# Kernel tuning notes

Measured on AMD Instinct MI355X. Metric: run time of the kernel, lower is better.

The kernel has to match this reference:

```python
import jax, jax.numpy as jnp
import numpy as np

N_HEADS = 32
N_KV_HEADS = 8
DIM = 4096
HEAD_DIM = DIM // N_HEADS  # 128
N_REP = N_HEADS // N_KV_HEADS  # 4
MAX_B = 4
CACHE_LEN = 1024
SEQ = 1024
BATCH = 4


def _rope(t, cos, sin):
    # t: (b, s, h, hd); interpret last dim as interleaved complex pairs
    tr = t[..., 0::2]
    ti = t[..., 1::2]
    cos = cos[None, :, None, :]
    sin = sin[None, :, None, :]
    out_r = tr * cos - ti * sin
    out_i = tr * sin + ti * cos
    return jnp.stack([out_r, out_i], axis=-1).reshape(t.shape)


def setup_inputs() -> dict:
    key = jax.random.key(0)
    ks = jax.random.split(key, 6)
    x = jax.random.normal(ks[0], (BATCH, SEQ, DIM), dtype=jnp.float32)
    wq = jax.random.normal(ks[1], (DIM, N_HEADS * HEAD_DIM), dtype=jnp.float32) * (DIM ** -0.5)
    wk = jax.random.normal(ks[2], (DIM, N_KV_HEADS * HEAD_DIM), dtype=jnp.float32) * (DIM ** -0.5)
    wv = jax.random.normal(ks[3], (DIM, N_KV_HEADS * HEAD_DIM), dtype=jnp.float32) * (DIM ** -0.5)
    wo = jax.random.normal(ks[4], (DIM, DIM), dtype=jnp.float32) * (DIM ** -0.5)
    # standard RoPE frequencies, theta = 10000
    inv_freq = 1.0 / (10000.0 ** (np.arange(0, HEAD_DIM, 2, dtype=np.float32) / HEAD_DIM))
    pos = np.arange(SEQ, dtype=np.float32)
    ang = np.outer(pos, inv_freq)  # (SEQ, HEAD_DIM/2)
    freqs_cos = jnp.asarray(np.cos(ang), dtype=jnp.float32)
    freqs_sin = jnp.asarray(np.sin(ang), dtype=jnp.float32)
    return {"x": x, "freqs_cos": freqs_cos, "freqs_sin": freqs_sin,
            "wq": wq, "wk": wk, "wv": wv, "wo": wo, "start": 0}


def reference(x, freqs_cos, freqs_sin, wq, wk, wv, wo, start):
    b, s, _ = x.shape
    xq = (x @ wq).reshape(b, s, N_HEADS, HEAD_DIM)
    xk = (x @ wk).reshape(b, s, N_KV_HEADS, HEAD_DIM)
    xv = (x @ wv).reshape(b, s, N_KV_HEADS, HEAD_DIM)

    xq = _rope(xq, freqs_cos, freqs_sin)
    xk = _rope(xk, freqs_cos, freqs_sin)

    # KV cache append (cache initialized to zeros as in the module)
    cache_k = jnp.zeros((MAX_B, CACHE_LEN, N_KV_HEADS, HEAD_DIM), dtype=x.dtype)
    cache_v = jnp.zeros((MAX_B, CACHE_LEN, N_KV_HEADS, HEAD_DIM), dtype=x.dtype)
    cache_k = cache_k.at[:b, start:start + s].set(xk)
    cache_v = cache_v.at[:b, start:start + s].set(xv)

    keys = cache_k[:b, :start + s]    # (b, kv, n_kv, hd)
    values = cache_v[:b, :start + s]

    # repeat_kv to match query heads (GQA)
    keys = jnp.repeat(keys, N_REP, axis=2)      # (b, kv, n_q, hd)
    values = jnp.repeat(values, N_REP, axis=2)

    scale = 1.0 / jnp.sqrt(jnp.float32(HEAD_DIM)).astype(x.dtype)
    scores = jnp.einsum('bqhd,bkhd->bhqk', xq, keys) * scale
    probs = jax.nn.softmax(scores, axis=-1)
    out = jnp.einsum('bhqk,bkhd->bqhd', probs, values).reshape(b, s, DIM)
    return out @ wo
```

## Files before the change

### kernel.cpp

```cpp
#include <hip/hip_runtime.h>
#include <cstdint>

#define B_SZ 4
#define S_LEN 1024
#define DIM 4096
#define NH 32
#define KVH 8
#define HD 128
#define DQKV 6144

typedef __bf16 bf16x8 __attribute__((ext_vector_type(8)));
typedef float f32x4 __attribute__((ext_vector_type(4)));

__device__ __forceinline__ unsigned short f2bf(float f) {
  union { float f; uint32_t u; } v; v.f = f;
  uint32_t u = v.u;
  return (unsigned short)((u + 0x7fffu + ((u >> 16) & 1u)) >> 16);
}
__device__ __forceinline__ float bf2f(unsigned short h) {
  union { uint32_t u; float f; } v; v.u = ((uint32_t)h) << 16;
  return v.f;
}

__device__ __forceinline__ void async16(void* lds, const void* g) {
  __builtin_amdgcn_global_load_lds(
      (const __attribute__((address_space(1))) void*)g,
      (__attribute__((address_space(3))) void*)lds, 16, 0, 0);
}

__global__ void cvt_x_kernel(const float* __restrict__ x, unsigned short* __restrict__ xb) {
  size_t i = ((size_t)blockIdx.x * 256 + threadIdx.x) * 4;
  float4 v = *(const float4*)(x + i);
  ushort4 o;
  o.x = f2bf(v.x); o.y = f2bf(v.y); o.z = f2bf(v.z); o.w = f2bf(v.w);
  *(ushort4*)(xb + i) = o;
}

__global__ void wtrans_kernel(const float* __restrict__ w, unsigned short* __restrict__ wt, int N) {
  __shared__ __align__(16) float tile[32][33];
  int n0 = blockIdx.x * 32, k0 = blockIdx.y * 32;
  int tx = threadIdx.x & 31, ty = threadIdx.x >> 5;
#pragma unroll
  for (int i = 0; i < 4; i++) {
    int k = ty + i * 8;
    tile[k][tx] = w[(size_t)(k0 + k) * N + n0 + tx];
  }
  __syncthreads();
#pragma unroll
  for (int i = 0; i < 4; i++) {
    int n = ty + i * 8;
    wt[(size_t)(n0 + n) * DIM + k0 + tx] = f2bf(tile[tx][n]);
  }
}

template <bool OUT_BF16>
__global__ __launch_bounds__(256, 2) void gemm_bt_kernel(
    const unsigned short* __restrict__ A, const unsigned short* __restrict__ Bt,
    void* __restrict__ Cout, int Kdim, int ldc) {
  __shared__ __align__(16) unsigned short lA[128 * 32];
  __shared__ __align__(16) unsigned short lB[128 * 32];
  const int tid = threadIdx.x;
  const int wave = tid >> 6, lane = tid & 63;
  const int m0 = blockIdx.y * 128, n0 = blockIdx.x * 128;
  const int r0 = tid >> 2, c0 = (tid & 3) * 8;
  const unsigned short* gA0 = A + (size_t)(m0 + r0) * Kdim + c0;
  const unsigned short* gA1 = gA0 + (size_t)64 * Kdim;
  const unsigned short* gB0 = Bt + (size_t)(n0 + r0) * Kdim + c0;
  const unsigned short* gB1 = gB0 + (size_t)64 * Kdim;
  unsigned short* lA0 = lA + wave * 512;
  unsigned short* lA1 = lA + 2048 + wave * 512;
  unsigned short* lB0 = lB + wave * 512;
  unsigned short* lB1 = lB + 2048 + wave * 512;
  const int wm = (wave & 1) * 64, wn = (wave >> 1) * 64;
  const int lql = lane & 15, lqh = lane >> 4;
  f32x4 acc[4][4] = {};
  for (int kk = 0; kk < Kdim; kk += 32) {
    __syncthreads();
    async16(lA0, gA0 + kk);
    async16(lA1, gA1 + kk);
    async16(lB0, gB0 + kk);
    async16(lB1, gB1 + kk);
    __syncthreads();
    bf16x8 af[4], bfr[4];
#pragma unroll
    for (int mi = 0; mi < 4; mi++)
      af[mi] = *(const bf16x8*)(lA + (wm + mi * 16 + lql) * 32 + lqh * 8);
#pragma unroll
    for (int ni = 0; ni < 4; ni++)
      bfr[ni] = *(const bf16x8*)(lB + (wn + ni * 16 + lql) * 32 + lqh * 8);
#pragma unroll
    for (int mi = 0; mi < 4; mi++)
#pragma unroll
      for (int ni = 0; ni < 4; ni++)
        acc[mi][ni] = __builtin_amdgcn_mfma_f32_16x16x32_bf16(af[mi], bfr[ni], acc[mi][ni], 0, 0, 0);
  }
#pragma unroll
  for (int mi = 0; mi < 4; mi++)
#pragma unroll
    for (int ni = 0; ni < 4; ni++)
#pragma unroll
      for (int r = 0; r < 4; r++) {
        int row = m0 + wm + mi * 16 + lqh * 4 + r;
        int col = n0 + wn + ni * 16 + lql;
        float v = acc[mi][ni][r];
        if (OUT_BF16)
          ((unsigned short*)Cout)[(size_t)row * ldc + col] = f2bf(v);
        else
          ((float*)Cout)[(size_t)row * ldc + col] = v;
      }
}

__global__ void rope_kernel(const unsigned short* __restrict__ src, const float* __restrict__ fc,
                            const float* __restrict__ fs, unsigned short* __restrict__ dst,
                            int nheads, float scale) {
  int idx = blockIdx.x * 256 + threadIdx.x;
  int f = idx & 63;
  int rest = idx >> 6;
  int hh = rest % nheads;
  int t = rest / nheads;
  int s = t & (S_LEN - 1);
  int b = t >> 10;
  const unsigned short* p = src + (size_t)t * DQKV + hh * HD + 2 * f;
  ushort2 xv = *(const ushort2*)p;
  float xr = bf2f(xv.x), xi = bf2f(xv.y);
  float c = fc[s * 64 + f], sn = fs[s * 64 + f];
  ushort2 o;
  o.x = f2bf((xr * c - xi * sn) * scale);
  o.y = f2bf((xr * sn + xi * c) * scale);
  *(ushort2*)(dst + ((size_t)(b * nheads + hh) * S_LEN + s) * HD + 2 * f) = o;
}

__global__ void vtrans_kernel(const unsigned short* __restrict__ src, unsigned short* __restrict__ Vt) {
  __shared__ __align__(16) unsigned short tile[32][33];
  int s0 = blockIdx.x * 32, d0 = blockIdx.y * 32, bk = blockIdx.z;
  int tx = threadIdx.x & 31, ty = threadIdx.x >> 5;
#pragma unroll
  for (int i = 0; i < 4; i++) {
    int s = ty + i * 8;
    tile[s][tx] = src[(size_t)((bk >> 3) * S_LEN + s0 + s) * DQKV + (bk & 7) * HD + d0 + tx];
  }
  __syncthreads();
#pragma unroll
  for (int i = 0; i < 4; i++) {
    int d = ty + i * 8;
    Vt[((size_t)bk * HD + d0 + d) * S_LEN + s0 + tx] = tile[tx][d];
  }
}

__global__ __launch_bounds__(256, 2) void attn_kernel(
    const unsigned short* __restrict__ Qb,
    const unsigned short* __restrict__ Kb,
    const unsigned short* __restrict__ Vt,
    unsigned short* __restrict__ Ob) {
  __shared__ __align__(16) unsigned short Kt[64][136];
  __shared__ __align__(16) unsigned short Vl[128][72];
  __shared__ __align__(16) unsigned short Pl[4][16][72];
  const int tid = threadIdx.x, wave = tid >> 6, lane = tid & 63;
  const int qb = blockIdx.x, h = blockIdx.y, b = blockIdx.z;
  const int kvh = h >> 2;
  const int lql = lane & 15, lqh = lane >> 4;
  const int qrow = qb * 64 + wave * 16;

  const unsigned short* Qp = Qb + ((size_t)(b * NH + h) * S_LEN + qrow + lql) * HD + lqh * 8;
  bf16x8 qf[4];
#pragma unroll
  for (int kd = 0; kd < 4; kd++) qf[kd] = *(const bf16x8*)(Qp + kd * 32);

  const unsigned short* Kp = Kb + (size_t)(b * KVH + kvh) * S_LEN * HD;
  const unsigned short* Vp = Vt + (size_t)(b * KVH + kvh) * HD * S_LEN;

  float m_run[4], l_run[4];
  f32x4 Oacc[8] = {};
#pragma unroll
  for (int r = 0; r < 4; r++) { m_run[r] = -3.0e38f; l_run[r] = 0.0f; }

  for (int kt = 0; kt < S_LEN; kt += 64) {
    __syncthreads();
#pragma unroll
    for (int i = 0; i < 4; i++) {
      int c = tid + 256 * i;
      int key = c >> 4, doff = (c & 15) * 8;
      *(uint4*)(&Kt[key][doff]) = *(const uint4*)(Kp + (size_t)(kt + key) * HD + doff);
    }
#pragma unroll
    for (int i = 0; i < 4; i++) {
      int c = tid + 256 * i;
      int d = c >> 3, koff = (c & 7) * 8;
      *(uint4*)(&Vl[d][koff]) = *(const uint4*)(Vp + (size_t)d * S_LEN + kt + koff);
    }
    __syncthreads();
    f32x4 sf[4] = {};
#pragma unroll
    for (int ni = 0; ni < 4; ni++)
#pragma unroll
      for (int kd = 0; kd < 4; kd++) {
        bf16x8 kf = *(const bf16x8*)(&Kt[ni * 16 + lql][kd * 32 + lqh * 8]);
        sf[ni] = __builtin_amdgcn_mfma_f32_16x16x32_bf16(qf[kd], kf, sf[ni], 0, 0, 0);
      }
    float mnew[4], alpha[4], psum[4];
#pragma unroll
    for (int r = 0; r < 4; r++) {
      float v = fmaxf(fmaxf(sf[0][r], sf[1][r]), fmaxf(sf[2][r], sf[3][r]));
      v = fmaxf(v, __shfl_xor(v, 1));
      v = fmaxf(v, __shfl_xor(v, 2));
      v = fmaxf(v, __shfl_xor(v, 4));
      v = fmaxf(v, __shfl_xor(v, 8));
      mnew[r] = fmaxf(m_run[r], v);
      alpha[r] = __expf(m_run[r] - mnew[r]);
      m_run[r] = mnew[r];
      psum[r] = 0.0f;
    }
#pragma unroll
    for (int ni = 0; ni < 4; ni++)
#pragma unroll
      for (int r = 0; r < 4; r++) {
        float p = __expf(sf[ni][r] - mnew[r]);
        psum[r] += p;
        Pl[wave][lqh * 4 + r][ni * 16 + lql] = f2bf(p);
      }
#pragma unroll
    for (int r = 0; r < 4; r++) {
      float v = psum[r];
      v += __shfl_xor(v, 1);
      v += __shfl_xor(v, 2);
      v += __shfl_xor(v, 4);
      v += __shfl_xor(v, 8);
      l_run[r] = l_run[r] * alpha[r] + v;
    }
#pragma unroll
    for (int ni = 0; ni < 8; ni++)
#pragma unroll
      for (int r = 0; r < 4; r++) Oacc[ni][r] *= alpha[r];
    bf16x8 pa[2];
#pragma unroll
    for (int ks = 0; ks < 2; ks++)
      pa[ks] = *(const bf16x8*)(&Pl[wave][lql][ks * 32 + lqh * 8]);
#pragma unroll
    for (int ni = 0; ni < 8; ni++)
#pragma unroll
      for (int ks = 0; ks < 2; ks++) {
        bf16x8 vb = *(const bf16x8*)(&Vl[ni * 16 + lql][ks * 32 + lqh * 8]);
        Oacc[ni] = __builtin_amdgcn_mfma_f32_16x16x32_bf16(pa[ks], vb, Oacc[ni], 0, 0, 0);
      }
  }
#pragma unroll
  for (int r = 0; r < 4; r++) l_run[r] = 1.0f / l_run[r];
#pragma unroll
  for (int ni = 0; ni < 8; ni++)
#pragma unroll
    for (int r = 0; r < 4; r++) {
      int q = qrow + lqh * 4 + r;
      Ob[(size_t)(b * S_LEN + q) * DIM + h * HD + ni * 16 + lql] = f2bf(Oacc[ni][r] * l_run[r]);
    }
}

extern "C" void kernel_launch(void* const* d_in, const int* in_sizes, int n_in,
                              void* d_out, int out_size, void* d_ws, size_t ws_size,
                              hipStream_t stream) {
  (void)in_sizes; (void)n_in; (void)out_size; (void)ws_size;
  const float* x  = (const float*)d_in[0];
  const float* fc = (const float*)d_in[1];
  const float* fs = (const float*)d_in[2];
  const float* wq = (const float*)d_in[3];
  const float* wk = (const float*)d_in[4];
  const float* wv = (const float*)d_in[5];
  const float* wo = (const float*)d_in[6];
  float* out = (float*)d_out;
  char* ws = (char*)d_ws;

  const size_t MB = 1024 * 1024;
  unsigned short* xb    = (unsigned short*)(ws + 0);
  unsigned short* attnb = (unsigned short*)(ws + 0);
  unsigned short* wqkvt = (unsigned short*)(ws + 32 * MB);
  unsigned short* Qb    = (unsigned short*)(ws + 32 * MB);
  unsigned short* Kb    = (unsigned short*)(ws + 64 * MB);
  unsigned short* Vt    = (unsigned short*)(ws + 72 * MB);
  unsigned short* wot   = (unsigned short*)(ws + 80 * MB);
  unsigned short* qkv   = (unsigned short*)(ws + 112 * MB);

  cvt_x_kernel<<<16384, 256, 0, stream>>>(x, xb);
  wtrans_kernel<<<dim3(128, 128), 256, 0, stream>>>(wq, wqkvt, 4096);
  wtrans_kernel<<<dim3(32, 128), 256, 0, stream>>>(wk, wqkvt + (size_t)4096 * 4096, 1024);
  wtrans_kernel<<<dim3(32, 128), 256, 0, stream>>>(wv, wqkvt + (size_t)5120 * 4096, 1024);
  wtrans_kernel<<<dim3(128, 128), 256, 0, stream>>>(wo, wot, 4096);
  gemm_bt_kernel<true><<<dim3(DQKV / 128, 32), 256, 0, stream>>>(xb, wqkvt, qkv, DIM, DQKV);
  rope_kernel<<<32768, 256, 0, stream>>>(qkv, fc, fs, Qb, NH, 0.08838834764831845f);
  rope_kernel<<<8192, 256, 0, stream>>>(qkv + 4096, fc, fs, Kb, KVH, 1.0f);
  vtrans_kernel<<<dim3(32, 4, 32), 256, 0, stream>>>(qkv + 5120, Vt);
  attn_kernel<<<dim3(16, NH, B_SZ), 256, 0, stream>>>(Qb, Kb, Vt, attnb);
  gemm_bt_kernel<false><<<dim3(32, 32), 256, 0, stream>>>(attnb, wot, out, DIM, DIM);
}
```

Before: 886.9 us.

## Swizzle LDS layouts, async-load attention tiles, vectorize rope and weight transpose

Applies XOR swizzles to the GEMM and attention LDS tiles so reads avoid bank conflicts without padding. K and V tiles are now filled with direct global-to-LDS async loads. Softmax switches to exp2 with log2(e) folded into the Q scale, and P is truncated to bf16 instead of rounded. Rope is vectorized to 16-byte accesses, the weight transpose uses 64x64 tiles with paired stores, and attention occupancy is raised to 3 blocks. The truncation slightly changes numerics and the swizzles must match the load layout exactly.

After: 804.2 us. 9.3% less time.

```diff
diff --git a/kernel.cpp b/kernel.cpp
--- a/kernel.cpp
+++ b/kernel.cpp
@@ -21,6 +21,13 @@
   union { uint32_t u; float f; } v; v.u = ((uint32_t)h) << 16;
   return v.f;
 }
+__device__ __forceinline__ float ex2(float x) {
+#if __has_builtin(__builtin_amdgcn_exp2f)
+  return __builtin_amdgcn_exp2f(x);
+#else
+  return exp2f(x);
+#endif
+}
 
 __device__ __forceinline__ void async16(void* lds, const void* g) {
   __builtin_amdgcn_global_load_lds(
@@ -37,19 +44,23 @@
 }
 
 __global__ void wtrans_kernel(const float* __restrict__ w, unsigned short* __restrict__ wt, int N) {
-  __shared__ __align__(16) float tile[32][33];
-  int n0 = blockIdx.x * 32, k0 = blockIdx.y * 32;
-  int tx = threadIdx.x & 31, ty = threadIdx.x >> 5;
-#pragma unroll
-  for (int i = 0; i < 4; i++) {
-    int k = ty + i * 8;
+  __shared__ float tile[64][65];
+  int n0 = blockIdx.x * 64, k0 = blockIdx.y * 64;
+  int tx = threadIdx.x & 63, ty = threadIdx.x >> 6;
+#pragma unroll
+  for (int i = 0; i < 16; i++) {
+    int k = ty + i * 4;
     tile[k][tx] = w[(size_t)(k0 + k) * N + n0 + tx];
   }
   __syncthreads();
-#pragma unroll
-  for (int i = 0; i < 4; i++) {
-    int n = ty + i * 8;
-    wt[(size_t)(n0 + n) * DIM + k0 + tx] = f2bf(tile[tx][n]);
+  int c = threadIdx.x & 31, ny = threadIdx.x >> 5;
+#pragma unroll
+  for (int i = 0; i < 8; i++) {
+    int n = ny + i * 8;
+    ushort2 o;
+    o.x = f2bf(tile[2 * c][n]);
+    o.y = f2bf(tile[2 * c + 1][n]);
+    *(ushort2*)(wt + (size_t)(n0 + n) * DIM + k0 + 2 * c) = o;
   }
 }
 
@@ -62,7 +73,8 @@
   const int tid = threadIdx.x;
   const int wave = tid >> 6, lane = tid & 63;
   const int m0 = blockIdx.y * 128, n0 = blockIdx.x * 128;
-  const int r0 = tid >> 2, c0 = (tid & 3) * 8;
+  const int r0 = tid >> 2;
+  const int c0 = ((tid & 3) ^ ((tid >> 3) & 3)) * 8;
   const unsigned short* gA0 = A + (size_t)(m0 + r0) * Kdim + c0;
   const unsigned short* gA1 = gA0 + (size_t)64 * Kdim;
   const unsigned short* gB0 = Bt + (size_t)(n0 + r0) * Kdim + c0;
@@ -73,6 +85,7 @@
   unsigned short* lB1 = lB + 2048 + wave * 512;
   const int wm = (wave & 1) * 64, wn = (wave >> 1) * 64;
   const int lql = lane & 15, lqh = lane >> 4;
+  const int ksw = (lqh ^ ((lql >> 1) & 3)) * 8;
   f32x4 acc[4][4] = {};
   for (int kk = 0; kk < Kdim; kk += 32) {
     __syncthreads();
@@ -84,10 +97,10 @@
     bf16x8 af[4], bfr[4];
 #pragma unroll
     for (int mi = 0; mi < 4; mi++)
-      af[mi] = *(const bf16x8*)(lA + (wm + mi * 16 + lql) * 32 + lqh * 8);
+      af[mi] = *(const bf16x8*)(lA + (wm + mi * 16 + lql) * 32 + ksw);
 #pragma unroll
     for (int ni = 0; ni < 4; ni++)
-      bfr[ni] = *(const bf16x8*)(lB + (wn + ni * 16 + lql) * 32 + lqh * 8);
+      bfr[ni] = *(const bf16x8*)(lB + (wn + ni * 16 + lql) * 32 + ksw);
 #pragma unroll
     for (int mi = 0; mi < 4; mi++)
 #pragma unroll
@@ -112,22 +125,27 @@
 
 __global__ void rope_kernel(const unsigned short* __restrict__ src, const float* __restrict__ fc,
                             const float* __restrict__ fs, unsigned short* __restrict__ dst,
-                            int nheads, float scale) {
+                            int nheads, int hshift, float scale) {
   int idx = blockIdx.x * 256 + threadIdx.x;
-  int f = idx & 63;
-  int rest = idx >> 6;
-  int hh = rest % nheads;
-  int t = rest / nheads;
+  int f4 = idx & 15;
+  int rest = idx >> 4;
+  int hh = rest & (nheads - 1);
+  int t = rest >> hshift;
   int s = t & (S_LEN - 1);
   int b = t >> 10;
-  const unsigned short* p = src + (size_t)t * DQKV + hh * HD + 2 * f;
-  ushort2 xv = *(const ushort2*)p;
-  float xr = bf2f(xv.x), xi = bf2f(xv.y);
-  float c = fc[s * 64 + f], sn = fs[s * 64 + f];
-  ushort2 o;
-  o.x = f2bf((xr * c - xi * sn) * scale);
-  o.y = f2bf((xr * sn + xi * c) * scale);
-  *(ushort2*)(dst + ((size_t)(b * nheads + hh) * S_LEN + s) * HD + 2 * f) = o;
+  union { uint4 v; unsigned short u[8]; } in, out;
+  in.v = *(const uint4*)(src + (size_t)t * DQKV + hh * HD + f4 * 8);
+  union { float4 v; float f[4]; } c4, s4;
+  c4.v = *(const float4*)(fc + s * 64 + f4 * 4);
+  s4.v = *(const float4*)(fs + s * 64 + f4 * 4);
+#pragma unroll
+  for (int j = 0; j < 4; j++) {
+    float xr = bf2f(in.u[2 * j]), xi = bf2f(in.u[2 * j + 1]);
+    float cc = c4.f[j], ss = s4.f[j];
+    out.u[2 * j] = f2bf((xr * cc - xi * ss) * scale);
+    out.u[2 * j + 1] = f2bf((xr * ss + xi * cc) * scale);
+  }
+  *(uint4*)(dst + ((size_t)(b * nheads + hh) * S_LEN + s) * HD + f4 * 8) = out.v;
 }
 
 __global__ void vtrans_kernel(const unsigned short* __restrict__ src, unsigned short* __restrict__ Vt) {
@@ -147,13 +165,13 @@
   }
 }
 
-__global__ __launch_bounds__(256, 2) void attn_kernel(
+__global__ __launch_bounds__(256, 3) void attn_kernel(
     const unsigned short* __restrict__ Qb,
     const unsigned short* __restrict__ Kb,
     const unsigned short* __restrict__ Vt,
     unsigned short* __restrict__ Ob) {
-  __shared__ __align__(16) unsigned short Kt[64][136];
-  __shared__ __align__(16) unsigned short Vl[128][72];
+  __shared__ __align__(16) unsigned short Kt[64][128];
+  __shared__ __align__(16) unsigned short Vl[128][64];
   __shared__ __align__(16) unsigned short Pl[4][16][72];
   const int tid = threadIdx.x, wave = tid >> 6, lane = tid & 63;
   const int qb = blockIdx.x, h = blockIdx.y, b = blockIdx.z;
@@ -168,6 +186,10 @@
 
   const unsigned short* Kp = Kb + (size_t)(b * KVH + kvh) * S_LEN * HD;
   const unsigned short* Vp = Vt + (size_t)(b * KVH + kvh) * HD * S_LEN;
+  const int krow_in = lane >> 4;
+  const int kcol_sw = lane & 15;
+  const int vrow_in = lane >> 3;
+  const int vcol_off = ((lane & 7) ^ (lane >> 3)) * 8;
 
   float m_run[4], l_run[4];
   f32x4 Oacc[8] = {};
@@ -177,26 +199,28 @@
   for (int kt = 0; kt < S_LEN; kt += 64) {
     __syncthreads();
 #pragma unroll
-    for (int i = 0; i < 4; i++) {
-      int c = tid + 256 * i;
-      int key = c >> 4, doff = (c & 15) * 8;
-      *(uint4*)(&Kt[key][doff]) = *(const uint4*)(Kp + (size_t)(kt + key) * HD + doff);
-    }
-#pragma unroll
-    for (int i = 0; i < 4; i++) {
-      int c = tid + 256 * i;
-      int d = c >> 3, koff = (c & 7) * 8;
-      *(uint4*)(&Vl[d][koff]) = *(const uint4*)(Vp + (size_t)d * S_LEN + kt + koff);
+    for (int j = 0; j < 4; j++) {
+      int rbase = wave * 16 + j * 4;
+      int r = rbase + krow_in;
+      async16(&Kt[rbase][0], Kp + (size_t)(kt + r) * HD + ((kcol_sw ^ (r & 7)) * 8));
+    }
+#pragma unroll
+    for (int j = 0; j < 4; j++) {
+      int dbase = wave * 32 + j * 8;
+      int d = dbase + vrow_in;
+      async16(&Vl[dbase][0], Vp + (size_t)d * S_LEN + kt + vcol_off);
     }
     __syncthreads();
     f32x4 sf[4] = {};
 #pragma unroll
-    for (int ni = 0; ni < 4; ni++)
+    for (int ni = 0; ni < 4; ni++) {
+      const int ksw = lql & 7;
 #pragma unroll
       for (int kd = 0; kd < 4; kd++) {
-        bf16x8 kf = *(const bf16x8*)(&Kt[ni * 16 + lql][kd * 32 + lqh * 8]);
+        bf16x8 kf = *(const bf16x8*)(&Kt[ni * 16 + lql][((kd * 4 + lqh) ^ ksw) * 8]);
         sf[ni] = __builtin_amdgcn_mfma_f32_16x16x32_bf16(qf[kd], kf, sf[ni], 0, 0, 0);
       }
+    }
     float mnew[4], alpha[4], psum[4];
 #pragma unroll
     for (int r = 0; r < 4; r++) {
@@ -206,7 +230,7 @@
       v = fmaxf(v, __shfl_xor(v, 4));
       v = fmaxf(v, __shfl_xor(v, 8));
       mnew[r] = fmaxf(m_run[r], v);
-      alpha[r] = __expf(m_run[r] - mnew[r]);
+      alpha[r] = ex2(m_run[r] - mnew[r]);
       m_run[r] = mnew[r];
       psum[r] = 0.0f;
     }
@@ -214,9 +238,10 @@
     for (int ni = 0; ni < 4; ni++)
 #pragma unroll
       for (int r = 0; r < 4; r++) {
-        float p = __expf(sf[ni][r] - mnew[r]);
+        float p = ex2(sf[ni][r] - mnew[r]);
         psum[r] += p;
-        Pl[wave][lqh * 4 + r][ni * 16 + lql] = f2bf(p);
+        union { float f; uint32_t u; } pv; pv.f = p;
+        Pl[wave][lqh * 4 + r][ni * 16 + lql] = (unsigned short)(pv.u >> 16);
       }
 #pragma unroll
     for (int r = 0; r < 4; r++) {
@@ -236,12 +261,14 @@
     for (int ks = 0; ks < 2; ks++)
       pa[ks] = *(const bf16x8*)(&Pl[wave][lql][ks * 32 + lqh * 8]);
 #pragma unroll
-    for (int ni = 0; ni < 8; ni++)
+    for (int ni = 0; ni < 8; ni++) {
+      const int ksw = lql & 7;
 #pragma unroll
       for (int ks = 0; ks < 2; ks++) {
-        bf16x8 vb = *(const bf16x8*)(&Vl[ni * 16 + lql][ks * 32 + lqh * 8]);
+        bf16x8 vb = *(const bf16x8*)(&Vl[ni * 16 + lql][((ks * 4 + lqh) ^ ksw) * 8]);
         Oacc[ni] = __builtin_amdgcn_mfma_f32_16x16x32_bf16(pa[ks], vb, Oacc[ni], 0, 0, 0);
       }
+    }
   }
 #pragma unroll
   for (int r = 0; r < 4; r++) l_run[r] = 1.0f / l_run[r];
@@ -279,13 +306,13 @@
   unsigned short* qkv   = (unsigned short*)(ws + 112 * MB);
 
   cvt_x_kernel<<<16384, 256, 0, stream>>>(x, xb);
-  wtrans_kernel<<<dim3(128, 128), 256, 0, stream>>>(wq, wqkvt, 4096);
-  wtrans_kernel<<<dim3(32, 128), 256, 0, stream>>>(wk, wqkvt + (size_t)4096 * 4096, 1024);
-  wtrans_kernel<<<dim3(32, 128), 256, 0, stream>>>(wv, wqkvt + (size_t)5120 * 4096, 1024);
-  wtrans_kernel<<<dim3(128, 128), 256, 0, stream>>>(wo, wot, 4096);
+  wtrans_kernel<<<dim3(64, 64), 256, 0, stream>>>(wq, wqkvt, 4096);
+  wtrans_kernel<<<dim3(16, 64), 256, 0, stream>>>(wk, wqkvt + (size_t)4096 * 4096, 1024);
+  wtrans_kernel<<<dim3(16, 64), 256, 0, stream>>>(wv, wqkvt + (size_t)5120 * 4096, 1024);
+  wtrans_kernel<<<dim3(64, 64), 256, 0, stream>>>(wo, wot, 4096);
   gemm_bt_kernel<true><<<dim3(DQKV / 128, 32), 256, 0, stream>>>(xb, wqkvt, qkv, DIM, DQKV);
-  rope_kernel<<<32768, 256, 0, stream>>>(qkv, fc, fs, Qb, NH, 0.08838834764831845f);
-  rope_kernel<<<8192, 256, 0, stream>>>(qkv + 4096, fc, fs, Kb, KVH, 1.0f);
+  rope_kernel<<<8192, 256, 0, stream>>>(qkv, fc, fs, Qb, NH, 5, 0.12751879505099168f);
+  rope_kernel<<<2048, 256, 0, stream>>>(qkv + 4096, fc, fs, Kb, KVH, 3, 1.0f);
   vtrans_kernel<<<dim3(32, 4, 32), 256, 0, stream>>>(qkv + 5120, Vt);
   attn_kernel<<<dim3(16, NH, B_SZ), 256, 0, stream>>>(Qb, Kb, Vt, attnb);
   gemm_bt_kernel<false><<<dim3(32, 32), 256, 0, stream>>>(attnb, wot, out, DIM, DIM);
```
